# Optimization experiments

Measured on AMD Instinct MI355X. Metric: run time of the kernel, lower is better.

## Reference

```python
import jax, jax.numpy as jnp
import numpy as np

HEADS = 4
DIM_HEAD = 32


def setup_inputs() -> dict:
    key = jax.random.key(0)
    k1, k2, k3 = jax.random.split(key, 3)
    b, dim, h, w = 16, 256, 64, 64
    hidden = HEADS * DIM_HEAD  # 128
    x = jax.random.normal(k1, (b, dim, h, w), dtype=jnp.float32)
    # 1x1 convs are just channel matmuls; store kernels as 2D matrices.
    W_qkv = jax.random.normal(k2, (3 * hidden, dim), dtype=jnp.float32) * 0.02
    W_out = jax.random.normal(k3, (dim, hidden), dtype=jnp.float32) * 0.02
    b_out = jnp.zeros((dim,), dtype=jnp.float32)
    return {"x": x, "W_qkv": W_qkv, "W_out": W_out, "b_out": b_out}


def reference(x, W_qkv, W_out, b_out):
    b, c, h, w = x.shape
    n = h * w
    # 1x1 conv: (b, 3*hidden, h, w) -> view (b, 3, heads, dim_head, n)
    qkv = jnp.einsum('bchw,oc->bohw', x, W_qkv)
    qkv = qkv.reshape(b, 3, HEADS, DIM_HEAD, n)
    q, k, v = qkv[:, 0], qkv[:, 1], qkv[:, 2]  # each (b, heads, dim_head, n)
    k = jax.nn.softmax(k, axis=-1)
    # context: (b, heads, dim_head, dim_head)
    context = jnp.einsum('bhdn,bhen->bhde', k, v)
    # out: (b, heads, dim_head, n)
    out = jnp.einsum('bhde,bhen->bhdn', context, q)
    out = out.reshape(b, HEADS * DIM_HEAD, h, w)
    # to_out 1x1 conv with bias
    y = jnp.einsum('bchw,oc->bohw', out, W_out) + b_out[None, :, None, None]
    return y
```

## Files before the change

### kernel.cpp

```cpp
#include <hip/hip_runtime.h>

typedef __attribute__((ext_vector_type(8))) short short8;
typedef __attribute__((ext_vector_type(4))) float f32x4;
typedef unsigned short u16;
typedef unsigned int u32;


__device__ __forceinline__ u16 f2bf(float f) {
    u32 x = __float_as_uint(f);
    u32 r = (x + 0x7fffu + ((x >> 16) & 1u)) >> 16;
    return (u16)r;
}
__device__ __forceinline__ float bf2f(u16 h) {
    return __uint_as_float(((u32)h) << 16);
}

typedef __attribute__((address_space(1))) u32 as1_u32;
typedef __attribute__((address_space(3))) u32 as3_u32;
__device__ __forceinline__ void gload16(const void* g, void* l) {
    __builtin_amdgcn_global_load_lds((as1_u32*)g, (as3_u32*)l, 16, 0, 0);
}

__global__ __launch_bounds__(256) void k_convW(const float* __restrict__ W,
                                               u16* __restrict__ Wb) {
    int idx = blockIdx.x * 256 + threadIdx.x;
    float4 v = *reinterpret_cast<const float4*>(W + idx * 4);
    u32 w0 = (u32)f2bf(v.x) | ((u32)f2bf(v.y) << 16);
    u32 w1 = (u32)f2bf(v.z) | ((u32)f2bf(v.w) << 16);
    uint2 o = {w0, w1};
    *reinterpret_cast<uint2*>(Wb + idx * 4) = o;
}

__global__ __launch_bounds__(256) void k_transpose(const float* __restrict__ x,
                                                   u16* __restrict__ xT) {
    __shared__ alignas(16) u16 tile[64 * 72];
    int t = threadIdx.x;
    int n0 = blockIdx.x * 64, c0 = blockIdx.y * 64, b = blockIdx.z;
    int rr = t >> 4, nq = (t & 15) * 4;
#pragma unroll
    for (int i = 0; i < 4; i++) {
        int cl = i * 16 + rr;
        float4 v = *reinterpret_cast<const float4*>(x + ((size_t)(b * 256 + c0 + cl) * 4096 + n0 + nq));
        u32 w0 = (u32)f2bf(v.x) | ((u32)f2bf(v.y) << 16);
        u32 w1 = (u32)f2bf(v.z) | ((u32)f2bf(v.w) << 16);
        uint2 o = {w0, w1};
        *reinterpret_cast<uint2*>(&tile[cl * 72 + nq]) = o;
    }
    __syncthreads();
    int r = t >> 3, c8 = (t & 7) * 8;
#pragma unroll
    for (int i = 0; i < 2; i++) {
        int nl = i * 32 + r;
        alignas(16) u16 vals[8];
#pragma unroll
        for (int j = 0; j < 8; j++) vals[j] = tile[(c8 + j) * 72 + nl];
        *reinterpret_cast<uint4*>(xT + ((size_t)(b * 4096 + n0 + nl) * 256 + c0 + c8)) =
            *reinterpret_cast<const uint4*>(vals);
    }
}

__global__ __launch_bounds__(256) void k_kv(const u16* __restrict__ xT,
                                            const u16* __restrict__ W,
                                            u16* __restrict__ kb,
                                            u16* __restrict__ vb) {
    __shared__ alignas(16) u16 sA[128 * 64];
    __shared__ alignas(16) u16 sB[128 * 64];
    int t = threadIdx.x;
    int mt = blockIdx.x, n0 = blockIdx.y * 128, b = blockIdx.z;
    int m0 = 128 + mt * 128;
    int lane = t & 63, wv = t >> 6, l16 = lane & 15, lq = lane >> 4;
    int wr = wv >> 1, wc = wv & 1;
    int trow = t >> 3, tc8 = (t & 7) * 8;

    f32x4 acc[4][4];
#pragma unroll
    for (int i = 0; i < 4; i++)
#pragma unroll
        for (int j = 0; j < 4; j++) acc[i][j] = (f32x4){0.f, 0.f, 0.f, 0.f};

    const u16* Asrc = W + (size_t)m0 * 256;
    const u16* Bsrc = xT + (size_t)(b * 4096 + n0) * 256;

    for (int kc = 0; kc < 4; kc++) {
        __syncthreads();
#pragma unroll
        for (int q = 0; q < 4; q++) {
            int row = q * 32 + trow;
            gload16(Asrc + (size_t)row * 256 + kc * 64 + tc8, &sA[row * 64 + tc8]);
            gload16(Bsrc + (size_t)row * 256 + kc * 64 + tc8, &sB[row * 64 + tc8]);
        }
        __syncthreads();
#pragma unroll
        for (int ks = 0; ks < 2; ks++) {
            int col = ks * 32 + lq * 8;
            short8 af[4], bfr[4];
#pragma unroll
            for (int i = 0; i < 4; i++)
                af[i] = *reinterpret_cast<const short8*>(&sA[(wr * 64 + i * 16 + l16) * 64 + col]);
#pragma unroll
            for (int j = 0; j < 4; j++)
                bfr[j] = *reinterpret_cast<const short8*>(&sB[(wc * 64 + j * 16 + l16) * 64 + col]);
#pragma unroll
            for (int i = 0; i < 4; i++)
#pragma unroll
                for (int j = 0; j < 4; j++)
                    acc[i][j] = __builtin_amdgcn_mfma_f32_16x16x32_bf16(af[i], bfr[j], acc[i][j], 0, 0, 0);
        }
    }
    u16* dst = (mt == 0) ? kb : vb;
#pragma unroll
    for (int i = 0; i < 4; i++) {
        int obase = wr * 64 + i * 16 + lq * 4;
#pragma unroll
        for (int j = 0; j < 4; j++) {
            int n = n0 + wc * 64 + j * 16 + l16;
            f32x4 a = acc[i][j];
#pragma unroll
            for (int rr = 0; rr < 4; rr++)
                dst[(size_t)(b * 128 + obase + rr) * 4096 + n] = f2bf(a[rr]);
        }
    }
}

__global__ __launch_bounds__(256) void k_ctx(const u16* __restrict__ kb,
                                             const u16* __restrict__ vb,
                                             float* __restrict__ part,
                                             float* __restrict__ denp) {
    __shared__ float sred[4][32][32];
    __shared__ float dls[4][32];
    int s = blockIdx.x, h = blockIdx.y, b = blockIdx.z;
    int t = threadIdx.x;
    int lane = t & 63, wv = t >> 6, l16 = lane & 15, lq = lane >> 4;
    int bh = b * 4 + h;
    const u16* Kb = kb + (size_t)(b * 128 + h * 32) * 4096;
    const u16* Vb = vb + (size_t)(b * 128 + h * 32) * 4096;
    int nb = s * 512 + wv * 128;

    f32x4 acc[2][2];
#pragma unroll
    for (int i = 0; i < 2; i++)
#pragma unroll
        for (int j = 0; j < 2; j++) acc[i][j] = (f32x4){0.f, 0.f, 0.f, 0.f};
    float s0 = 0.f, s1 = 0.f;

#pragma unroll
    for (int kk = 0; kk < 4; kk++) {
        int col = nb + kk * 32 + lq * 8;
        short8 af[2], bfr[2];
#pragma unroll
        for (int i = 0; i < 2; i++) {
            short8 raw = *reinterpret_cast<const short8*>(Kb + (size_t)(i * 16 + l16) * 4096 + col);
            short8 pf;
            float ssum = 0.f;
#pragma unroll
            for (int e = 0; e < 8; e++) {
                float ef = __expf(bf2f((u16)raw[e]));
                ssum += ef;
                pf[e] = (short)f2bf(ef);
            }
            if (i == 0) s0 += ssum; else s1 += ssum;
            af[i] = pf;
        }
#pragma unroll
        for (int j = 0; j < 2; j++)
            bfr[j] = *reinterpret_cast<const short8*>(Vb + (size_t)(j * 16 + l16) * 4096 + col);
#pragma unroll
        for (int i = 0; i < 2; i++)
#pragma unroll
            for (int j = 0; j < 2; j++)
                acc[i][j] = __builtin_amdgcn_mfma_f32_16x16x32_bf16(af[i], bfr[j], acc[i][j], 0, 0, 0);
    }
    s0 += __shfl_xor(s0, 16, 64); s0 += __shfl_xor(s0, 32, 64);
    s1 += __shfl_xor(s1, 16, 64); s1 += __shfl_xor(s1, 32, 64);
    if (lane < 16) { dls[wv][l16] = s0; dls[wv][16 + l16] = s1; }
#pragma unroll
    for (int i = 0; i < 2; i++)
#pragma unroll
        for (int j = 0; j < 2; j++)
#pragma unroll
            for (int rr = 0; rr < 4; rr++)
                sred[wv][i * 16 + lq * 4 + rr][j * 16 + l16] = acc[i][j][rr];
    __syncthreads();
    if (t < 32) {
        float d = dls[0][t] + dls[1][t] + dls[2][t] + dls[3][t];
        denp[(size_t)(bh * 8 + s) * 32 + t] = d;
    }
    int de0 = t * 4;
    const float* p0 = &sred[0][0][0];
    f32x4 sum;
#pragma unroll
    for (int q = 0; q < 4; q++)
        sum[q] = p0[de0 + q] + p0[1024 + de0 + q] + p0[2048 + de0 + q] + p0[3072 + de0 + q];
    *reinterpret_cast<f32x4*>(part + (size_t)(bh * 8 + s) * 1024 + de0) = sum;
}

__global__ __launch_bounds__(256) void k_red(const float* __restrict__ part,
                                             const float* __restrict__ denp,
                                             float* __restrict__ C) {
    __shared__ float invd[32];
    int bh = blockIdx.x, t = threadIdx.x;
    if (t < 32) {
        float d = 0.f;
#pragma unroll
        for (int s = 0; s < 8; s++) d += denp[(size_t)(bh * 8 + s) * 32 + t];
        invd[t] = 1.0f / d;
    }
    __syncthreads();
    int de0 = t * 4;
    float a0 = 0.f, a1 = 0.f, a2 = 0.f, a3 = 0.f;
#pragma unroll
    for (int s = 0; s < 8; s++) {
        f32x4 v = *reinterpret_cast<const f32x4*>(part + (size_t)(bh * 8 + s) * 1024 + de0);
        a0 += v[0]; a1 += v[1]; a2 += v[2]; a3 += v[3];
    }
    float iv = invd[de0 >> 5];
    f32x4 o = {a0 * iv, a1 * iv, a2 * iv, a3 * iv};
    *reinterpret_cast<f32x4*>(C + (size_t)bh * 1024 + de0) = o;
}

__global__ __launch_bounds__(256) void k_G(const float* __restrict__ C,
                                           const float* __restrict__ Wout,
                                           const float* __restrict__ Wqkv,
                                           u16* __restrict__ Gb) {
    __shared__ float Cs[4096];
    __shared__ float Us[2048];
    int b = blockIdx.x, ot = blockIdx.y, t = threadIdx.x;
    int o0 = ot * 16;
#pragma unroll
    for (int q = 0; q < 16; q++) {
        int idx = q * 256 + t;
        Cs[idx] = C[(size_t)b * 4096 + idx];
    }
    __syncthreads();
#pragma unroll
    for (int q = 0; q < 8; q++) {
        int idx = q * 256 + t;
        int ol = idx >> 7, he = idx & 127;
        int h = he >> 5, e = he & 31;
        const float* wrow = Wout + (o0 + ol) * 128 + h * 32;
        const float* crow = &Cs[h * 1024 + e];
        float a = 0.f;
#pragma unroll
        for (int d = 0; d < 32; d++) a += wrow[d] * crow[d * 32];
        Us[idx] = a;
    }
    __syncthreads();
    int ol = t >> 4, c0 = (t & 15) * 16;
    float acc[16];
#pragma unroll
    for (int cc = 0; cc < 16; cc++) acc[cc] = 0.f;
    const float* Ur = &Us[ol * 128];
#pragma unroll 4
    for (int he = 0; he < 128; he++) {
        float u = Ur[he];
        const float4* wq = reinterpret_cast<const float4*>(Wqkv + he * 256 + c0);
#pragma unroll
        for (int q4 = 0; q4 < 4; q4++) {
            float4 w = wq[q4];
            acc[q4 * 4 + 0] += u * w.x;
            acc[q4 * 4 + 1] += u * w.y;
            acc[q4 * 4 + 2] += u * w.z;
            acc[q4 * 4 + 3] += u * w.w;
        }
    }
    alignas(16) u16 ob[16];
#pragma unroll
    for (int cc = 0; cc < 16; cc++) ob[cc] = f2bf(acc[cc]);
    u16* dst = Gb + (size_t)(b * 256 + o0 + ol) * 256 + c0;
    *reinterpret_cast<uint4*>(dst) = *reinterpret_cast<const uint4*>(ob);
    *reinterpret_cast<uint4*>(dst + 8) = *reinterpret_cast<const uint4*>(ob + 8);
}

__global__ __launch_bounds__(256) void k_y(const u16* __restrict__ Gb,
                                           const u16* __restrict__ xT,
                                           const float* __restrict__ bout,
                                           float* __restrict__ y) {
    __shared__ alignas(16) u16 sA[128 * 64];
    __shared__ alignas(16) u16 sB[128 * 64];
    int t = threadIdx.x;
    int mt = blockIdx.x, n0 = blockIdx.y * 128, b = blockIdx.z;
    int m0 = mt * 128;
    int lane = t & 63, wv = t >> 6, l16 = lane & 15, lq = lane >> 4;
    int wr = wv >> 1, wc = wv & 1;
    int trow = t >> 3, tc8 = (t & 7) * 8;

    f32x4 acc[4][4];
#pragma unroll
    for (int i = 0; i < 4; i++)
#pragma unroll
        for (int j = 0; j < 4; j++) acc[i][j] = (f32x4){0.f, 0.f, 0.f, 0.f};

    const u16* Asrc = Gb + (size_t)(b * 256 + m0) * 256;
    const u16* Bsrc = xT + (size_t)(b * 4096 + n0) * 256;

    for (int kc = 0; kc < 4; kc++) {
        __syncthreads();
#pragma unroll
        for (int q = 0; q < 4; q++) {
            int row = q * 32 + trow;
            gload16(Asrc + (size_t)row * 256 + kc * 64 + tc8, &sA[row * 64 + tc8]);
            gload16(Bsrc + (size_t)row * 256 + kc * 64 + tc8, &sB[row * 64 + tc8]);
        }
        __syncthreads();
#pragma unroll
        for (int ks = 0; ks < 2; ks++) {
            int col = ks * 32 + lq * 8;
            short8 af[4], bfr[4];
#pragma unroll
            for (int i = 0; i < 4; i++)
                af[i] = *reinterpret_cast<const short8*>(&sA[(wr * 64 + i * 16 + l16) * 64 + col]);
#pragma unroll
            for (int j = 0; j < 4; j++)
                bfr[j] = *reinterpret_cast<const short8*>(&sB[(wc * 64 + j * 16 + l16) * 64 + col]);
#pragma unroll
            for (int i = 0; i < 4; i++)
#pragma unroll
                for (int j = 0; j < 4; j++)
                    acc[i][j] = __builtin_amdgcn_mfma_f32_16x16x32_bf16(af[i], bfr[j], acc[i][j], 0, 0, 0);
        }
    }
#pragma unroll
    for (int i = 0; i < 4; i++) {
        int obase = m0 + wr * 64 + i * 16 + lq * 4;
#pragma unroll
        for (int j = 0; j < 4; j++) {
            int n = n0 + wc * 64 + j * 16 + l16;
#pragma unroll
            for (int rr = 0; rr < 4; rr++) {
                int o = obase + rr;
                y[(size_t)(b * 256 + o) * 4096 + n] = acc[i][j][rr] + bout[o];
            }
        }
    }
}

extern "C" void kernel_launch(void* const* d_in, const int* in_sizes, int n_in,
                              void* d_out, int out_size, void* d_ws, size_t ws_size,
                              hipStream_t stream) {
    const float* x    = (const float*)d_in[0];
    const float* Wqkv = (const float*)d_in[1];
    const float* Wout = (const float*)d_in[2];
    const float* bout = (const float*)d_in[3];
    float* y = (float*)d_out;

    u16* kb = (u16*)d_out;
    u16* vb = (u16*)d_out + 8388608;

    char* ws = (char*)d_ws;
    u16*   xT   = (u16*)(ws);
    float* part = (float*)(ws + 33554432);
    float* denp = (float*)(ws + 35651584);
    float* C    = (float*)(ws + 35717120);
    u16*   Gb   = (u16*)(ws + 35979264);
    u16*   Wb   = (u16*)(ws + 38076416);

    k_convW    <<<96, 256, 0, stream>>>(Wqkv, Wb);
    k_transpose<<<dim3(64, 4, 16), 256, 0, stream>>>(x, xT);
    k_kv       <<<dim3(2, 32, 16), 256, 0, stream>>>(xT, Wb, kb, vb);
    k_ctx      <<<dim3(8, 4, 16), 256, 0, stream>>>(kb, vb, part, denp);
    k_red      <<<64, 256, 0, stream>>>(part, denp, C);
    k_G        <<<dim3(16, 16), 256, 0, stream>>>(C, Wout, Wqkv, Gb);
    k_y        <<<dim3(2, 32, 16), 256, 0, stream>>>(Gb, xT, bout, y);
}
```

Measured before the change: 197.4 us.

## Fuse transpose, K/V projection, softmax-exp and context into one kernel

Merges the weight conversion, x transpose to bf16, K/V 1x1 projection and per-tile context accumulation into a single 512-thread kernel that keeps the transposed x tile in swizzled LDS. K and V no longer round-trip through global memory: exp(K) and V are written to LDS and multiplied directly, producing per-tile partial contexts and denominators. The reduction kernel now sums 32 tile partials instead of 8. This cuts kernel launches and about 32MB of K/V traffic, at the cost of ~100KB LDS per block (one block per CU) and more partial data to reduce.

```diff
diff --git a/kernel.cpp b/kernel.cpp
--- a/kernel.cpp
+++ b/kernel.cpp
@@ -11,9 +11,6 @@
     u32 r = (x + 0x7fffu + ((x >> 16) & 1u)) >> 16;
     return (u16)r;
 }
-__device__ __forceinline__ float bf2f(u16 h) {
-    return __uint_as_float(((u32)h) << 16);
-}
 
 typedef __attribute__((address_space(1))) u32 as1_u32;
 typedef __attribute__((address_space(3))) u32 as3_u32;
@@ -21,56 +18,46 @@
     __builtin_amdgcn_global_load_lds((as1_u32*)g, (as3_u32*)l, 16, 0, 0);
 }
 
-__global__ __launch_bounds__(256) void k_convW(const float* __restrict__ W,
-                                               u16* __restrict__ Wb) {
-    int idx = blockIdx.x * 256 + threadIdx.x;
-    float4 v = *reinterpret_cast<const float4*>(W + idx * 4);
-    u32 w0 = (u32)f2bf(v.x) | ((u32)f2bf(v.y) << 16);
-    u32 w1 = (u32)f2bf(v.z) | ((u32)f2bf(v.w) << 16);
-    uint2 o = {w0, w1};
-    *reinterpret_cast<uint2*>(Wb + idx * 4) = o;
-}
-
-__global__ __launch_bounds__(256) void k_transpose(const float* __restrict__ x,
-                                                   u16* __restrict__ xT) {
-    __shared__ alignas(16) u16 tile[64 * 72];
+__global__ __launch_bounds__(512) void k_fused(const float* __restrict__ x,
+                                               const float* __restrict__ Wqkv,
+                                               u16* __restrict__ xT,
+                                               float* __restrict__ part,
+                                               float* __restrict__ denp) {
+    __shared__ alignas(16) char smem[104448];
+    u16* sB = (u16*)smem;
+    u16* sA = (u16*)(smem + 67584);
+    u16* Pl = (u16*)smem;
+    u16* Vl = (u16*)(smem + 34816);
+    float* dpart = (float*)(smem + 69632);
+
     int t = threadIdx.x;
-    int n0 = blockIdx.x * 64, c0 = blockIdx.y * 64, b = blockIdx.z;
-    int rr = t >> 4, nq = (t & 15) * 4;
-#pragma unroll
-    for (int i = 0; i < 4; i++) {
-        int cl = i * 16 + rr;
-        float4 v = *reinterpret_cast<const float4*>(x + ((size_t)(b * 256 + c0 + cl) * 4096 + n0 + nq));
-        u32 w0 = (u32)f2bf(v.x) | ((u32)f2bf(v.y) << 16);
-        u32 w1 = (u32)f2bf(v.z) | ((u32)f2bf(v.w) << 16);
-        uint2 o = {w0, w1};
-        *reinterpret_cast<uint2*>(&tile[cl * 72 + nq]) = o;
-    }
-    __syncthreads();
-    int r = t >> 3, c8 = (t & 7) * 8;
-#pragma unroll
-    for (int i = 0; i < 2; i++) {
-        int nl = i * 32 + r;
-        alignas(16) u16 vals[8];
-#pragma unroll
-        for (int j = 0; j < 8; j++) vals[j] = tile[(c8 + j) * 72 + nl];
-        *reinterpret_cast<uint4*>(xT + ((size_t)(b * 4096 + n0 + nl) * 256 + c0 + c8)) =
-            *reinterpret_cast<const uint4*>(vals);
-    }
-}
-
-__global__ __launch_bounds__(256) void k_kv(const u16* __restrict__ xT,
-                                            const u16* __restrict__ W,
-                                            u16* __restrict__ kb,
-                                            u16* __restrict__ vb) {
-    __shared__ alignas(16) u16 sA[128 * 64];
-    __shared__ alignas(16) u16 sB[128 * 64];
-    int t = threadIdx.x;
-    int mt = blockIdx.x, n0 = blockIdx.y * 128, b = blockIdx.z;
-    int m0 = 128 + mt * 128;
+    int nt = blockIdx.x, b = blockIdx.y;
+    int n0 = nt * 128;
     int lane = t & 63, wv = t >> 6, l16 = lane & 15, lq = lane >> 4;
     int wr = wv >> 1, wc = wv & 1;
-    int trow = t >> 3, tc8 = (t & 7) * 8;
+
+    for (int i = 0; i < 16; i++) {
+        int qi = i * 512 + t;
+        int cl = qi >> 5;
+        int nq = (qi & 31) * 4;
+        float4 v = *reinterpret_cast<const float4*>(x + ((size_t)(b * 256 + cl) * 4096 + n0 + nq));
+        float vv[4] = {v.x, v.y, v.z, v.w};
+#pragma unroll
+        for (int j = 0; j < 4; j++) {
+            int n = nq + j;
+            int cs = cl ^ (((n >> 3) & 7) << 3);
+            sB[n * 264 + cs] = f2bf(vv[j]);
+        }
+    }
+    __syncthreads();
+    for (int i = 0; i < 8; i++) {
+        int wi = i * 512 + t;
+        int nl = wi >> 5;
+        int cg = (wi & 31) * 8;
+        int cs = cg ^ (((nl >> 3) & 7) << 3);
+        uint4 vals = *reinterpret_cast<const uint4*>(&sB[nl * 264 + cs]);
+        *reinterpret_cast<uint4*>(xT + ((size_t)(b * 4096 + n0 + nl) * 256 + cg)) = vals;
+    }
 
     f32x4 acc[4][4];
 #pragma unroll
@@ -78,28 +65,34 @@
 #pragma unroll
         for (int j = 0; j < 4; j++) acc[i][j] = (f32x4){0.f, 0.f, 0.f, 0.f};
 
-    const u16* Asrc = W + (size_t)m0 * 256;
-    const u16* Bsrc = xT + (size_t)(b * 4096 + n0) * 256;
-
+    const float* Wsrc = Wqkv + 128 * 256;
     for (int kc = 0; kc < 4; kc++) {
         __syncthreads();
 #pragma unroll
-        for (int q = 0; q < 4; q++) {
-            int row = q * 32 + trow;
-            gload16(Asrc + (size_t)row * 256 + kc * 64 + tc8, &sA[row * 64 + tc8]);
-            gload16(Bsrc + (size_t)row * 256 + kc * 64 + tc8, &sB[row * 64 + tc8]);
+        for (int q = 0; q < 8; q++) {
+            int fi = q * 512 + t;
+            int row = fi >> 4, cq = (fi & 15) * 4;
+            float4 w = *reinterpret_cast<const float4*>(Wsrc + (size_t)row * 256 + kc * 64 + cq);
+            u32 w0 = (u32)f2bf(w.x) | ((u32)f2bf(w.y) << 16);
+            u32 w1 = (u32)f2bf(w.z) | ((u32)f2bf(w.w) << 16);
+            uint2 o = {w0, w1};
+            *reinterpret_cast<uint2*>(&sA[row * 72 + cq]) = o;
         }
         __syncthreads();
 #pragma unroll
         for (int ks = 0; ks < 2; ks++) {
-            int col = ks * 32 + lq * 8;
+            int colA = ks * 32 + lq * 8;
+            int colB = kc * 64 + ks * 32 + lq * 8;
             short8 af[4], bfr[4];
 #pragma unroll
             for (int i = 0; i < 4; i++)
-                af[i] = *reinterpret_cast<const short8*>(&sA[(wr * 64 + i * 16 + l16) * 64 + col]);
-#pragma unroll
-            for (int j = 0; j < 4; j++)
-                bfr[j] = *reinterpret_cast<const short8*>(&sB[(wc * 64 + j * 16 + l16) * 64 + col]);
+                af[i] = *reinterpret_cast<const short8*>(&sA[(wr * 64 + i * 16 + l16) * 72 + colA]);
+#pragma unroll
+            for (int j = 0; j < 4; j++) {
+                int n = wc * 64 + j * 16 + l16;
+                int cs = colB ^ (((n >> 3) & 7) << 3);
+                bfr[j] = *reinterpret_cast<const short8*>(&sB[n * 264 + cs]);
+            }
 #pragma unroll
             for (int i = 0; i < 4; i++)
 #pragma unroll
@@ -107,110 +100,91 @@
                     acc[i][j] = __builtin_amdgcn_mfma_f32_16x16x32_bf16(af[i], bfr[j], acc[i][j], 0, 0, 0);
         }
     }
-    u16* dst = (mt == 0) ? kb : vb;
-#pragma unroll
-    for (int i = 0; i < 4; i++) {
-        int obase = wr * 64 + i * 16 + lq * 4;
-#pragma unroll
-        for (int j = 0; j < 4; j++) {
-            int n = n0 + wc * 64 + j * 16 + l16;
-            f32x4 a = acc[i][j];
-#pragma unroll
-            for (int rr = 0; rr < 4; rr++)
-                dst[(size_t)(b * 128 + obase + rr) * 4096 + n] = f2bf(a[rr]);
-        }
-    }
-}
-
-__global__ __launch_bounds__(256) void k_ctx(const u16* __restrict__ kb,
-                                             const u16* __restrict__ vb,
-                                             float* __restrict__ part,
-                                             float* __restrict__ denp) {
-    __shared__ float sred[4][32][32];
-    __shared__ float dls[4][32];
-    int s = blockIdx.x, h = blockIdx.y, b = blockIdx.z;
-    int t = threadIdx.x;
-    int lane = t & 63, wv = t >> 6, l16 = lane & 15, lq = lane >> 4;
-    int bh = b * 4 + h;
-    const u16* Kb = kb + (size_t)(b * 128 + h * 32) * 4096;
-    const u16* Vb = vb + (size_t)(b * 128 + h * 32) * 4096;
-    int nb = s * 512 + wv * 128;
-
-    f32x4 acc[2][2];
+    __syncthreads();
+
+    if (wr < 2) {
+#pragma unroll
+        for (int i = 0; i < 4; i++) {
+            int rbase = wr * 64 + i * 16 + lq * 4;
+            float srow[4] = {0.f, 0.f, 0.f, 0.f};
+#pragma unroll
+            for (int j = 0; j < 4; j++) {
+                int n = wc * 64 + j * 16 + l16;
+#pragma unroll
+                for (int rr = 0; rr < 4; rr++) {
+                    float e = __expf(acc[i][j][rr]);
+                    Pl[(rbase + rr) * 136 + n] = f2bf(e);
+                    srow[rr] += e;
+                }
+            }
+#pragma unroll
+            for (int rr = 0; rr < 4; rr++) {
+                float s = srow[rr];
+                s += __shfl_xor(s, 1, 64); s += __shfl_xor(s, 2, 64);
+                s += __shfl_xor(s, 4, 64); s += __shfl_xor(s, 8, 64);
+                if (l16 == 0) dpart[(rbase + rr) * 2 + wc] = s;
+            }
+        }
+    } else {
+#pragma unroll
+        for (int i = 0; i < 4; i++) {
+            int rbase = (wr - 2) * 64 + i * 16 + lq * 4;
+#pragma unroll
+            for (int j = 0; j < 4; j++) {
+                int n = wc * 64 + j * 16 + l16;
+#pragma unroll
+                for (int rr = 0; rr < 4; rr++)
+                    Vl[(rbase + rr) * 136 + n] = f2bf(acc[i][j][rr]);
+            }
+        }
+    }
+    __syncthreads();
+
+    int h = wv >> 1, eh = wv & 1;
+    f32x4 a2[2];
+    a2[0] = (f32x4){0.f, 0.f, 0.f, 0.f};
+    a2[1] = (f32x4){0.f, 0.f, 0.f, 0.f};
+#pragma unroll
+    for (int kk = 0; kk < 4; kk++) {
+        int col = kk * 32 + lq * 8;
+        short8 bfr = *reinterpret_cast<const short8*>(&Vl[(h * 32 + eh * 16 + l16) * 136 + col]);
+#pragma unroll
+        for (int i = 0; i < 2; i++) {
+            short8 af = *reinterpret_cast<const short8*>(&Pl[(h * 32 + i * 16 + l16) * 136 + col]);
+            a2[i] = __builtin_amdgcn_mfma_f32_16x16x32_bf16(af, bfr, a2[i], 0, 0, 0);
+        }
+    }
+    float* pp = part + ((size_t)(b * 32 + nt) * 4 + h) * 1024;
 #pragma unroll
     for (int i = 0; i < 2; i++)
 #pragma unroll
-        for (int j = 0; j < 2; j++) acc[i][j] = (f32x4){0.f, 0.f, 0.f, 0.f};
-    float s0 = 0.f, s1 = 0.f;
-
-#pragma unroll
-    for (int kk = 0; kk < 4; kk++) {
-        int col = nb + kk * 32 + lq * 8;
-        short8 af[2], bfr[2];
-#pragma unroll
-        for (int i = 0; i < 2; i++) {
-            short8 raw = *reinterpret_cast<const short8*>(Kb + (size_t)(i * 16 + l16) * 4096 + col);
-            short8 pf;
-            float ssum = 0.f;
-#pragma unroll
-            for (int e = 0; e < 8; e++) {
-                float ef = __expf(bf2f((u16)raw[e]));
-                ssum += ef;
-                pf[e] = (short)f2bf(ef);
-            }
-            if (i == 0) s0 += ssum; else s1 += ssum;
-            af[i] = pf;
-        }
-#pragma unroll
-        for (int j = 0; j < 2; j++)
-            bfr[j] = *reinterpret_cast<const short8*>(Vb + (size_t)(j * 16 + l16) * 4096 + col);
-#pragma unroll
-        for (int i = 0; i < 2; i++)
-#pragma unroll
-            for (int j = 0; j < 2; j++)
-                acc[i][j] = __builtin_amdgcn_mfma_f32_16x16x32_bf16(af[i], bfr[j], acc[i][j], 0, 0, 0);
-    }
-    s0 += __shfl_xor(s0, 16, 64); s0 += __shfl_xor(s0, 32, 64);
-    s1 += __shfl_xor(s1, 16, 64); s1 += __shfl_xor(s1, 32, 64);
-    if (lane < 16) { dls[wv][l16] = s0; dls[wv][16 + l16] = s1; }
-#pragma unroll
-    for (int i = 0; i < 2; i++)
-#pragma unroll
-        for (int j = 0; j < 2; j++)
-#pragma unroll
-            for (int rr = 0; rr < 4; rr++)
-                sred[wv][i * 16 + lq * 4 + rr][j * 16 + l16] = acc[i][j][rr];
-    __syncthreads();
-    if (t < 32) {
-        float d = dls[0][t] + dls[1][t] + dls[2][t] + dls[3][t];
-        denp[(size_t)(bh * 8 + s) * 32 + t] = d;
-    }
-    int de0 = t * 4;
-    const float* p0 = &sred[0][0][0];
-    f32x4 sum;
-#pragma unroll
-    for (int q = 0; q < 4; q++)
-        sum[q] = p0[de0 + q] + p0[1024 + de0 + q] + p0[2048 + de0 + q] + p0[3072 + de0 + q];
-    *reinterpret_cast<f32x4*>(part + (size_t)(bh * 8 + s) * 1024 + de0) = sum;
+        for (int rr = 0; rr < 4; rr++)
+            pp[(i * 16 + lq * 4 + rr) * 32 + eh * 16 + l16] = a2[i][rr];
+
+    if (t < 128)
+        denp[((size_t)b * 128 + t) * 32 + nt] = dpart[t * 2] + dpart[t * 2 + 1];
 }
 
 __global__ __launch_bounds__(256) void k_red(const float* __restrict__ part,
                                              const float* __restrict__ denp,
                                              float* __restrict__ C) {
     __shared__ float invd[32];
-    int bh = blockIdx.x, t = threadIdx.x;
+    int bh = blockIdx.x;
+    int b = bh >> 2, h = bh & 3;
+    int t = threadIdx.x;
     if (t < 32) {
-        float d = 0.f;
-#pragma unroll
-        for (int s = 0; s < 8; s++) d += denp[(size_t)(bh * 8 + s) * 32 + t];
-        invd[t] = 1.0f / d;
+        const float* dp = denp + ((size_t)b * 128 + h * 32 + t) * 32;
+        float s = 0.f;
+#pragma unroll
+        for (int nt = 0; nt < 32; nt++) s += dp[nt];
+        invd[t] = 1.0f / s;
     }
     __syncthreads();
     int de0 = t * 4;
     float a0 = 0.f, a1 = 0.f, a2 = 0.f, a3 = 0.f;
-#pragma unroll
-    for (int s = 0; s < 8; s++) {
-        f32x4 v = *reinterpret_cast<const f32x4*>(part + (size_t)(bh * 8 + s) * 1024 + de0);
+#pragma unroll 8
+    for (int nt = 0; nt < 32; nt++) {
+        f32x4 v = *reinterpret_cast<const f32x4*>(part + ((size_t)(b * 32 + nt) * 4 + h) * 1024 + de0);
         a0 += v[0]; a1 += v[1]; a2 += v[2]; a3 += v[3];
     }
     float iv = invd[de0 >> 5];
@@ -343,22 +317,15 @@
     const float* bout = (const float*)d_in[3];
     float* y = (float*)d_out;
 
-    u16* kb = (u16*)d_out;
-    u16* vb = (u16*)d_out + 8388608;
-
     char* ws = (char*)d_ws;
     u16*   xT   = (u16*)(ws);
     float* part = (float*)(ws + 33554432);
-    float* denp = (float*)(ws + 35651584);
-    float* C    = (float*)(ws + 35717120);
-    u16*   Gb   = (u16*)(ws + 35979264);
-    u16*   Wb   = (u16*)(ws + 38076416);
-
-    k_convW    <<<96, 256, 0, stream>>>(Wqkv, Wb);
-    k_transpose<<<dim3(64, 4, 16), 256, 0, stream>>>(x, xT);
-    k_kv       <<<dim3(2, 32, 16), 256, 0, stream>>>(xT, Wb, kb, vb);
-    k_ctx      <<<dim3(8, 4, 16), 256, 0, stream>>>(kb, vb, part, denp);
-    k_red      <<<64, 256, 0, stream>>>(part, denp, C);
-    k_G        <<<dim3(16, 16), 256, 0, stream>>>(C, Wout, Wqkv, Gb);
-    k_y        <<<dim3(2, 32, 16), 256, 0, stream>>>(Gb, xT, bout, y);
-}
+    float* denp = (float*)(ws + 41943040);
+    float* C    = (float*)(ws + 42205184);
+    u16*   Gb   = (u16*)(ws + 42467328);
+
+    k_fused<<<dim3(32, 16), 512, 0, stream>>>(x, Wqkv, xT, part, denp);
+    k_red  <<<64, 256, 0, stream>>>(part, denp, C);
+    k_G    <<<dim3(16, 16), 256, 0, stream>>>(C, Wout, Wqkv, Gb);
+    k_y    <<<dim3(2, 32, 16), 256, 0, stream>>>(Gb, xT, bout, y);
+}
```

Result: faster. 193.5 us (-2.0%).
